# Kernel optimization log

Hardware: AMD Instinct MI355X
Metric: run time of the kernel (lower is better)

The kernel has to match this reference:

```python
import jax, jax.numpy as jnp
import numpy as np

TOKENS, IN_F, OUT_F = 32768, 512, 512
INIT_STD = 0.02


def _binarize(v):
    # straight-through sign: forward = sign(v), backward = d tanh(v)
    hard = jnp.where(v >= 0, jnp.ones_like(v), -jnp.ones_like(v))
    soft = jnp.tanh(v)
    return soft + jax.lax.stop_gradient(hard - soft)


def _round_ste(v):
    return v + jax.lax.stop_gradient(jnp.round(v) - v)


def _shift_scale(shift_param, lo=-8.0, hi=0.0):
    return 2.0 ** _round_ste(jnp.clip(shift_param, lo, hi))


def setup_inputs() -> dict:
    key = jax.random.key(0)
    kx, kw = jax.random.split(key, 2)
    x = jax.random.normal(kx, (TOKENS, IN_F), dtype=jnp.float32)
    weight = jax.random.normal(kw, (OUT_F, IN_F), dtype=jnp.float32) * INIT_STD
    threshold = jnp.zeros((OUT_F, 1), dtype=jnp.float32)
    shift_param = jnp.asarray(-4.5, dtype=jnp.float32)
    return {"x": x, "weight": weight, "threshold": threshold, "shift_param": shift_param}


def reference(x, weight, threshold, shift_param):
    x_q = _binarize(x)                       # [N, in]
    w_q = _binarize(weight - threshold)      # [out, in]
    out = jnp.einsum('ni,oi->no', x_q, w_q)  # F.linear
    return out * _shift_scale(shift_param)
```

## Files before the change

kernel.cpp:

```cpp
#include <hip/hip_runtime.h>
#include <stdint.h>

#define TOKENS 32768
#define IN_F   512
#define OUT_F  512
#define KW     16

typedef float f32x4 __attribute__((ext_vector_type(4)));


__global__ __launch_bounds__(256) void binw_kernel(
    const float* __restrict__ w,
    const float* __restrict__ thr,
    uint32_t* __restrict__ wbT)
{
    const int o    = (blockIdx.x * 256 + threadIdx.x) >> 6;
    const int lane = threadIdx.x & 63;

    const float t = thr[o];
    const float4* wr = (const float4*)(w + (size_t)o * IN_F);
#pragma unroll
    for (int j = 0; j < 2; ++j) {
        float4 v = wr[j * 64 + lane];
        float vals[4] = {v.x - t, v.y - t, v.z - t, v.w - t};
#pragma unroll
        for (int c = 0; c < 4; ++c) {
            unsigned long long m = __ballot(vals[c] >= 0.0f);
            if (lane == 0) {
                wbT[(j * 8 + c * 2 + 0) * OUT_F + o] = (uint32_t)m;
                wbT[(j * 8 + c * 2 + 1) * OUT_F + o] = (uint32_t)(m >> 32);
            }
        }
    }
}

__global__ __launch_bounds__(256, 4) void bgemm_kernel(
    const float*    __restrict__ x,
    const uint32_t* __restrict__ wbT,
    const float*    __restrict__ shift,
    float*          __restrict__ out)
{
    const int lane = threadIdx.x & 63;
    const int wid  = threadIdx.x >> 6;
    const int gw   = blockIdx.x * 4 + wid;
    const int og   = gw & 1;
    const int row_base = gw >> 1;

    uint32_t wv[KW][4];
    const uint32_t* wp = wbT + og * 256 + lane * 4;
#pragma unroll
    for (int k = 0; k < KW; ++k) {
        uint4 v = *(const uint4*)(wp + k * OUT_F);
        wv[k][0] = v.x; wv[k][1] = v.y; wv[k][2] = v.z; wv[k][3] = v.w;
    }

    float s = shift[0];
    s = fminf(fmaxf(s, -8.0f), 0.0f);
    const float scale   = exp2f(rintf(s));
    const float negtwos = -2.0f * scale;
    const float basev   = (float)IN_F * scale;

    const float4* xr = (const float4*)x;

    float4 a[2][2];
    a[0][0] = xr[(size_t)row_base * 128 + lane];
    a[0][1] = xr[(size_t)row_base * 128 + 64 + lane];
    a[1][0] = xr[(size_t)(row_base + 2048) * 128 + lane];
    a[1][1] = xr[(size_t)(row_base + 2048) * 128 + 64 + lane];

#pragma unroll
    for (int j = 0; j < 16; ++j) {
        const int slot = j & 1;
        const int row  = row_base + j * 2048;

        uint32_t xw[KW];
        {
            unsigned long long m;
            m = __ballot(a[slot][0].x >= 0.0f); xw[0]  = (uint32_t)m; xw[1]  = (uint32_t)(m >> 32);
            m = __ballot(a[slot][0].y >= 0.0f); xw[2]  = (uint32_t)m; xw[3]  = (uint32_t)(m >> 32);
            m = __ballot(a[slot][0].z >= 0.0f); xw[4]  = (uint32_t)m; xw[5]  = (uint32_t)(m >> 32);
            m = __ballot(a[slot][0].w >= 0.0f); xw[6]  = (uint32_t)m; xw[7]  = (uint32_t)(m >> 32);
            m = __ballot(a[slot][1].x >= 0.0f); xw[8]  = (uint32_t)m; xw[9]  = (uint32_t)(m >> 32);
            m = __ballot(a[slot][1].y >= 0.0f); xw[10] = (uint32_t)m; xw[11] = (uint32_t)(m >> 32);
            m = __ballot(a[slot][1].z >= 0.0f); xw[12] = (uint32_t)m; xw[13] = (uint32_t)(m >> 32);
            m = __ballot(a[slot][1].w >= 0.0f); xw[14] = (uint32_t)m; xw[15] = (uint32_t)(m >> 32);
        }

        if (j < 14) {
            const size_t nb = (size_t)(row + 4096) * 128;
            a[slot][0] = xr[nb + lane];
            a[slot][1] = xr[nb + 64 + lane];
        }

        uint32_t acc0 = 0, acc1 = 0, acc2 = 0, acc3 = 0;
#pragma unroll
        for (int k = 0; k < KW; ++k) {
            acc0 += __popc(xw[k] ^ wv[k][0]);
            acc1 += __popc(xw[k] ^ wv[k][1]);
            acc2 += __popc(xw[k] ^ wv[k][2]);
            acc3 += __popc(xw[k] ^ wv[k][3]);
        }

        f32x4 o4;
        o4.x = fmaf(negtwos, (float)acc0, basev);
        o4.y = fmaf(negtwos, (float)acc1, basev);
        o4.z = fmaf(negtwos, (float)acc2, basev);
        o4.w = fmaf(negtwos, (float)acc3, basev);
        __builtin_nontemporal_store(o4,
            (f32x4*)&out[(size_t)row * OUT_F + og * 256 + lane * 4]);
    }
}

extern "C" void kernel_launch(void* const* d_in, const int* in_sizes, int n_in,
                              void* d_out, int out_size, void* d_ws, size_t ws_size,
                              hipStream_t stream) {
    const float* x     = (const float*)d_in[0];
    const float* w     = (const float*)d_in[1];
    const float* thr   = (const float*)d_in[2];
    const float* shift = (const float*)d_in[3];
    float*       out   = (float*)d_out;
    uint32_t*    wbT   = (uint32_t*)d_ws;

    binw_kernel<<<128, 256, 0, stream>>>(w, thr, wbT);
    bgemm_kernel<<<1024, 256, 0, stream>>>(x, wbT, shift, out);
}
```

Before: 33.14 us.

## Pre-pack binarized x into bitmasks in a separate pass before the GEMM

The x binarization moves out of the GEMM kernel into a combined pack kernel that also packs the weights. Each row of x is written once as 16 uint32 words to the workspace. Before, each x row was read as fp32 by two wavefronts (one per output half), so x was loaded twice. The GEMM now reads 64-byte packed rows with uniform (broadcast) loads instead of full fp32 rows and no longer needs ballots. The cost is an extra write and read of the small packed buffer and a dependency between the two kernels.

Result: slower. 77.30 us (+133.3%).

```diff
diff --git a/kernel.cpp b/kernel.cpp
--- a/kernel.cpp
+++ b/kernel.cpp
@@ -9,33 +9,67 @@
 typedef float f32x4 __attribute__((ext_vector_type(4)));
 
 
-__global__ __launch_bounds__(256) void binw_kernel(
+__global__ __launch_bounds__(256) void pack_kernel(
+    const float* __restrict__ x,
     const float* __restrict__ w,
     const float* __restrict__ thr,
+    uint32_t* __restrict__ xb,
     uint32_t* __restrict__ wbT)
 {
-    const int o    = (blockIdx.x * 256 + threadIdx.x) >> 6;
     const int lane = threadIdx.x & 63;
+    const int wid  = threadIdx.x >> 6;
 
-    const float t = thr[o];
-    const float4* wr = (const float4*)(w + (size_t)o * IN_F);
+    if (blockIdx.x < 2048) {
+        const int g = blockIdx.x * 4 + wid;
+        const float4* xr = (const float4*)x;
 #pragma unroll
-    for (int j = 0; j < 2; ++j) {
-        float4 v = wr[j * 64 + lane];
-        float vals[4] = {v.x - t, v.y - t, v.z - t, v.w - t};
+        for (int r = 0; r < 4; ++r) {
+            const int row = g * 4 + r;
+            float4 v0 = xr[(size_t)row * 128 + lane];
+            float4 v1 = xr[(size_t)row * 128 + 64 + lane];
+            unsigned long long m0 = __ballot(v0.x >= 0.0f);
+            unsigned long long m1 = __ballot(v0.y >= 0.0f);
+            unsigned long long m2 = __ballot(v0.z >= 0.0f);
+            unsigned long long m3 = __ballot(v0.w >= 0.0f);
+            unsigned long long m4 = __ballot(v1.x >= 0.0f);
+            unsigned long long m5 = __ballot(v1.y >= 0.0f);
+            unsigned long long m6 = __ballot(v1.z >= 0.0f);
+            unsigned long long m7 = __ballot(v1.w >= 0.0f);
+            if (lane == 0) {
+                uint4* p = (uint4*)(xb + (size_t)row * KW);
+                uint4 q0 = {(uint32_t)m0, (uint32_t)(m0 >> 32),
+                            (uint32_t)m1, (uint32_t)(m1 >> 32)};
+                uint4 q1 = {(uint32_t)m2, (uint32_t)(m2 >> 32),
+                            (uint32_t)m3, (uint32_t)(m3 >> 32)};
+                uint4 q2 = {(uint32_t)m4, (uint32_t)(m4 >> 32),
+                            (uint32_t)m5, (uint32_t)(m5 >> 32)};
+                uint4 q3 = {(uint32_t)m6, (uint32_t)(m6 >> 32),
+                            (uint32_t)m7, (uint32_t)(m7 >> 32)};
+                p[0] = q0; p[1] = q1; p[2] = q2; p[3] = q3;
+            }
+        }
+    } else {
+        const int o = ((blockIdx.x - 2048) * 256 + (int)threadIdx.x) >> 6;
+        const float t = thr[o];
+        const float4* wr = (const float4*)(w + (size_t)o * IN_F);
 #pragma unroll
-        for (int c = 0; c < 4; ++c) {
-            unsigned long long m = __ballot(vals[c] >= 0.0f);
-            if (lane == 0) {
-                wbT[(j * 8 + c * 2 + 0) * OUT_F + o] = (uint32_t)m;
-                wbT[(j * 8 + c * 2 + 1) * OUT_F + o] = (uint32_t)(m >> 32);
+        for (int j = 0; j < 2; ++j) {
+            float4 v = wr[j * 64 + lane];
+            float vals[4] = {v.x - t, v.y - t, v.z - t, v.w - t};
+#pragma unroll
+            for (int c = 0; c < 4; ++c) {
+                unsigned long long m = __ballot(vals[c] >= 0.0f);
+                if (lane == 0) {
+                    wbT[(j * 8 + c * 2 + 0) * OUT_F + o] = (uint32_t)m;
+                    wbT[(j * 8 + c * 2 + 1) * OUT_F + o] = (uint32_t)(m >> 32);
+                }
             }
         }
     }
 }
 
 __global__ __launch_bounds__(256, 4) void bgemm_kernel(
-    const float*    __restrict__ x,
+    const uint32_t* __restrict__ xb,
     const uint32_t* __restrict__ wbT,
     const float*    __restrict__ shift,
     float*          __restrict__ out)
@@ -60,36 +94,29 @@
     const float negtwos = -2.0f * scale;
     const float basev   = (float)IN_F * scale;
 
-    const float4* xr = (const float4*)x;
+    const uint4* xbr = (const uint4*)xb;
 
-    float4 a[2][2];
-    a[0][0] = xr[(size_t)row_base * 128 + lane];
-    a[0][1] = xr[(size_t)row_base * 128 + 64 + lane];
-    a[1][0] = xr[(size_t)(row_base + 2048) * 128 + lane];
-    a[1][1] = xr[(size_t)(row_base + 2048) * 128 + 64 + lane];
+    uint4 a[2][4];
+#pragma unroll
+    for (int q = 0; q < 4; ++q) a[0][q] = xbr[(size_t)row_base * 4 + q];
+#pragma unroll
+    for (int q = 0; q < 4; ++q) a[1][q] = xbr[(size_t)(row_base + 2048) * 4 + q];
 
 #pragma unroll
     for (int j = 0; j < 16; ++j) {
         const int slot = j & 1;
         const int row  = row_base + j * 2048;
 
-        uint32_t xw[KW];
-        {
-            unsigned long long m;
-            m = __ballot(a[slot][0].x >= 0.0f); xw[0]  = (uint32_t)m; xw[1]  = (uint32_t)(m >> 32);
-            m = __ballot(a[slot][0].y >= 0.0f); xw[2]  = (uint32_t)m; xw[3]  = (uint32_t)(m >> 32);
-            m = __ballot(a[slot][0].z >= 0.0f); xw[4]  = (uint32_t)m; xw[5]  = (uint32_t)(m >> 32);
-            m = __ballot(a[slot][0].w >= 0.0f); xw[6]  = (uint32_t)m; xw[7]  = (uint32_t)(m >> 32);
-            m = __ballot(a[slot][1].x >= 0.0f); xw[8]  = (uint32_t)m; xw[9]  = (uint32_t)(m >> 32);
-            m = __ballot(a[slot][1].y >= 0.0f); xw[10] = (uint32_t)m; xw[11] = (uint32_t)(m >> 32);
-            m = __ballot(a[slot][1].z >= 0.0f); xw[12] = (uint32_t)m; xw[13] = (uint32_t)(m >> 32);
-            m = __ballot(a[slot][1].w >= 0.0f); xw[14] = (uint32_t)m; xw[15] = (uint32_t)(m >> 32);
-        }
+        uint32_t xw[KW] = {
+            a[slot][0].x, a[slot][0].y, a[slot][0].z, a[slot][0].w,
+            a[slot][1].x, a[slot][1].y, a[slot][1].z, a[slot][1].w,
+            a[slot][2].x, a[slot][2].y, a[slot][2].z, a[slot][2].w,
+            a[slot][3].x, a[slot][3].y, a[slot][3].z, a[slot][3].w};
 
         if (j < 14) {
-            const size_t nb = (size_t)(row + 4096) * 128;
-            a[slot][0] = xr[nb + lane];
-            a[slot][1] = xr[nb + 64 + lane];
+            const size_t nb = (size_t)(row + 4096) * 4;
+#pragma unroll
+            for (int q = 0; q < 4; ++q) a[slot][q] = xbr[nb + q];
         }
 
         uint32_t acc0 = 0, acc1 = 0, acc2 = 0, acc3 = 0;
@@ -119,8 +146,10 @@
     const float* thr   = (const float*)d_in[2];
     const float* shift = (const float*)d_in[3];
     float*       out   = (float*)d_out;
-    uint32_t*    wbT   = (uint32_t*)d_ws;
 
-    binw_kernel<<<128, 256, 0, stream>>>(w, thr, wbT);
-    bgemm_kernel<<<1024, 256, 0, stream>>>(x, wbT, shift, out);
+    uint32_t* wbT = (uint32_t*)d_ws;
+    uint32_t* xb  = (uint32_t*)((char*)d_ws + 32768);
+
+    pack_kernel<<<2048 + 128, 256, 0, stream>>>(x, w, thr, xb, wbT);
+    bgemm_kernel<<<1024, 256, 0, stream>>>(xb, wbT, shift, out);
 }
```
